# Kernel optimization log

Hardware: AMD Instinct MI355X
Metric: run time of the kernel (lower is better)

## Reference

```python
import jax, jax.numpy as jnp
import numpy as np

N_NODES = 100000
N_EDGES = 3200000
D = 128


def setup_inputs() -> dict:
    key = jax.random.key(0)
    k1, k2, k3, k4, k5 = jax.random.split(key, 5)
    x = jax.random.normal(k1, (N_NODES, D), dtype=jnp.float32)
    weight = jax.random.normal(k2, (D, D), dtype=jnp.float32) * (1.0 / np.sqrt(D))
    bias = jax.random.normal(k3, (D,), dtype=jnp.float32) * 0.01
    edge_weight = jax.random.uniform(k4, (N_EDGES,), dtype=jnp.float32)
    edge_index = jax.random.randint(k5, (2, N_EDGES), 0, N_NODES, dtype=jnp.int64 if jax.config.jax_enable_x64 else jnp.int32)
    return {"x": x, "weight": weight, "bias": bias,
            "edge_weight": edge_weight, "edge_index": edge_index}


def gcn_conv(x, weight, bias, edge_index, edge_weight):
    # PyG GCNConv defaults: normalize=True, add_self_loops=True (fill=1),
    # flow source_to_target: messages gathered from edge_index[0], scattered to edge_index[1].
    n = x.shape[0]
    src, dst = edge_index[0], edge_index[1]
    loop = jnp.arange(n, dtype=src.dtype)
    src = jnp.concatenate([src, loop])
    dst = jnp.concatenate([dst, loop])
    ew = jnp.concatenate([edge_weight, jnp.ones((n,), dtype=edge_weight.dtype)])
    deg = jax.ops.segment_sum(ew, dst, num_segments=n)          # [N]
    dinv = jnp.where(deg > 0, jax.lax.rsqrt(jnp.where(deg > 0, deg, 1.0)), 0.0)
    norm = dinv[src] * ew * dinv[dst]                           # [E+N]
    h = x @ weight.T                                            # [N, D_out]
    msg = h[src] * norm[:, None]                                # gather + scale
    out = jax.ops.segment_sum(msg, dst, num_segments=n)         # scatter-add
    return out + bias


def reference(x, weight, bias, edge_weight, edge_index):
    h = gcn_conv(x, weight, bias, edge_index, edge_weight)
    h = jax.nn.relu(h)            # normalizer is Identity, activation=F.relu
    h = h + x                     # input_dim == output_dim -> projection=Identity
    # dropout: eval mode (deterministic reference) -> no-op
    return h
```

## Files before the change

### kernel.cpp

```cpp
#include <hip/hip_runtime.h>

#define N_NODES 100000
#define N_EDGES 3200000
#define DIM 128

#define NB_C  98
#define CAP_C 36864
#define NB_F  1568
#define CAP_F 2560
#define CAP   96



__device__ __forceinline__ unsigned short f2bf(float f) {
    unsigned u = __float_as_uint(f);
    return (unsigned short)((u + 0x7fffu + ((u >> 16) & 1u)) >> 16);
}


__global__ __launch_bounds__(256) void zero_i_kernel(int* __restrict__ p, int n) {
    int i = blockIdx.x * 256 + threadIdx.x;
    if (i < n) p[i] = 0;
}

__global__ __launch_bounds__(256) void zero_f_kernel(float* __restrict__ p, int n) {
    int i = blockIdx.x * 256 + threadIdx.x;
    if (i < n) p[i] = 0.0f;
}

__global__ __launch_bounds__(256) void zero_u64_kernel(unsigned long long* __restrict__ p, int n) {
    int i = blockIdx.x * 256 + threadIdx.x;
    if (i < n) p[i] = 0ull;
}

__global__ __launch_bounds__(256) void zero_f4_kernel(float4* __restrict__ p, int n4) {
    int i = blockIdx.x * 256 + threadIdx.x;
    if (i < n4) p[i] = make_float4(0.f, 0.f, 0.f, 0.f);
}

__global__ __launch_bounds__(256) void dinv_kernel(float* __restrict__ deg) {
    int i = blockIdx.x * 256 + threadIdx.x;
    if (i < N_NODES) deg[i] = rsqrtf(deg[i] + 1.0f);
}

__global__ __launch_bounds__(256) void dinv_packed_kernel(const unsigned long long* __restrict__ packed,
                                                          float* __restrict__ dinv) {
    int i = blockIdx.x * 256 + threadIdx.x;
    if (i < N_NODES) {
        unsigned long long p = packed[i];
        float deg = (float)(p & 0xFFFFFFFFFFull) * (1.0f / 4294967296.0f);
        dinv[i] = rsqrtf(deg + 1.0f);
    }
}

__global__ __launch_bounds__(256) void wt_kernel(const float* __restrict__ W,
                                                 float* __restrict__ Wt) {
    int idx = blockIdx.x * 256 + threadIdx.x;
    int j = idx >> 7, k = idx & 127;
    Wt[k * 128 + j] = W[idx];
}


__global__ __launch_bounds__(256) void prep_kernel(const float* __restrict__ W,
                                                   float* __restrict__ Wt,
                                                   int* __restrict__ fills) {
    const int b = blockIdx.x;
    const int tid = threadIdx.x;
    if (b < 64) {
        int idx = b * 256 + tid;
        int j = idx >> 7, k = idx & 127;
        Wt[k * 128 + j] = W[idx];
    } else {
        int i = (b - 64) * 256 + tid;
        if (i < NB_C + NB_F) fills[i] = 0;
    }
}


__global__ __launch_bounds__(256) void xscale_kernel(const float4* __restrict__ x4,
                                                     const float* __restrict__ dinv,
                                                     ushort4* __restrict__ xh4) {
    const int i0 = blockIdx.x * 512 + threadIdx.x;
#pragma unroll
    for (int r = 0; r < 2; ++r) {
        int i = i0 + r * 256;
        float di = dinv[i >> 5];
        float4 v = x4[i];
        ushort4 h;
        h.x = f2bf(v.x * di); h.y = f2bf(v.y * di);
        h.z = f2bf(v.z * di); h.w = f2bf(v.w * di);
        xh4[i] = h;
    }
}


__global__ __launch_bounds__(256) void partA1_kernel(const int* __restrict__ ei,
                                                     const float* __restrict__ ew,
                                                     int* __restrict__ fill_c,
                                                     unsigned long long* __restrict__ edc) {
    __shared__ int hist[NB_C];
    __shared__ int base[NB_C];
    const int tid = threadIdx.x;
    const int blockbase = blockIdx.x * 4096;
    for (int i = tid; i < NB_C; i += 256) hist[i] = 0;
    __syncthreads();

    unsigned long long pay[16];
    unsigned meta[16];
#pragma unroll
    for (int i = 0; i < 16; ++i) {
        int e = blockbase + i * 256 + tid;
        meta[i] = 0xFFFFFFFFu;
        if (e < N_EDGES) {
            int src = ei[e];
            int dst = ei[N_EDGES + e];
            float w = ew[e];
            int cb = dst >> 10;
            int pos = atomicAdd(&hist[cb], 1);
            pay[i] = ((unsigned long long)__float_as_uint(w) << 32)
                   | ((unsigned)(dst & 1023) << 17) | (unsigned)src;
            meta[i] = ((unsigned)cb << 16) | (unsigned)pos;
        }
    }
    __syncthreads();
    for (int c = tid; c < NB_C; c += 256) {
        int cnt = hist[c];
        base[c] = (cnt > 0) ? atomicAdd(&fill_c[c], cnt) : 0;
    }
    __syncthreads();
#pragma unroll
    for (int i = 0; i < 16; ++i) {
        if (meta[i] != 0xFFFFFFFFu) {
            int cb = (int)(meta[i] >> 16);
            int pos = base[cb] + (int)(meta[i] & 0xFFFFu);
            if (pos < CAP_C)
                edc[(unsigned)cb * CAP_C + (unsigned)pos] = pay[i];
        }
    }
}


__global__ __launch_bounds__(256) void partA2_kernel(const int* __restrict__ fill_c,
                                                     const unsigned long long* __restrict__ edc,
                                                     int* __restrict__ fill_f,
                                                     unsigned long long* __restrict__ edf) {
    __shared__ int hist[16];
    __shared__ int base[16];
    const int tid = threadIdx.x;
    const int cb = blockIdx.x / 9;
    const int lo = (blockIdx.x % 9) * 4096;
    const int cnt_c = min(fill_c[cb], CAP_C);
    const int hi = min(lo + 4096, cnt_c);
    if (tid < 16) hist[tid] = 0;
    __syncthreads();

    unsigned long long pay[16];
    unsigned meta[16];
#pragma unroll
    for (int i = 0; i < 16; ++i) {
        int idx = lo + i * 256 + tid;
        meta[i] = 0xFFFFFFFFu;
        if (idx < hi) {
            unsigned long long p = edc[(unsigned)cb * CAP_C + (unsigned)idx];
            int f = (int)((p >> 23) & 15);
            int pos = atomicAdd(&hist[f], 1);
            pay[i] = p;
            meta[i] = ((unsigned)f << 16) | (unsigned)pos;
        }
    }
    __syncthreads();
    if (tid < 16) {
        int c = hist[tid];
        base[tid] = (c > 0) ? atomicAdd(&fill_f[cb * 16 + tid], c) : 0;
    }
    __syncthreads();
#pragma unroll
    for (int i = 0; i < 16; ++i) {
        if (meta[i] != 0xFFFFFFFFu) {
            int f = (int)(meta[i] >> 16);
            int pos = base[f] + (int)(meta[i] & 0xFFFFu);
            if (pos < CAP_F)
                edf[((unsigned)(cb * 16 + f)) * CAP_F + (unsigned)pos] = pay[i];
        }
    }
}


__global__ __launch_bounds__(256) void partB_kernel(const int* __restrict__ fill_f,
                                                    unsigned long long* __restrict__ edf,
                                                    float* __restrict__ dinv,
                                                    int* __restrict__ row_start,
                                                    int* __restrict__ row_cnt) {
    __shared__ int hist[64];
    __shared__ float degs[64];
    __shared__ int pref[64];
    const int tid = threadIdx.x;
    const int fb = blockIdx.x;
    const int node_base = (fb >> 4) * 1024 + (fb & 15) * 64;
    const int cnt = min(fill_f[fb], CAP_F);
    if (tid < 64) { hist[tid] = 0; degs[tid] = 0.0f; }
    __syncthreads();

    unsigned long long pay[10];
    unsigned meta[10];
    int m = 0;
    for (int idx = tid; idx < cnt; idx += 256) {
        unsigned long long p = edf[(unsigned)fb * CAP_F + (unsigned)idx];
        int dl = (int)((p >> 17) & 63);
        int pos = atomicAdd(&hist[dl], 1);
        atomicAdd(&degs[dl], __uint_as_float((unsigned)(p >> 32)));
        pay[m] = p;
        meta[m] = ((unsigned)dl << 16) | (unsigned)pos;
        ++m;
    }
    __syncthreads();
    if (tid == 0) {
        int run = 0;
#pragma unroll
        for (int n = 0; n < 64; ++n) { pref[n] = run; run += hist[n]; }
    }
    __syncthreads();
    if (tid < 64) {
        int node = node_base + tid;
        if (node < N_NODES) {
            dinv[node] = rsqrtf(degs[tid] + 1.0f);
            row_start[node] = fb * CAP_F + pref[tid];
            row_cnt[node] = hist[tid];
        }
    }
    for (int i = 0; i < m; ++i) {
        int dl = (int)(meta[i] >> 16);
        edf[(unsigned)fb * CAP_F + (unsigned)(pref[dl] + (int)(meta[i] & 0xFFFFu))] = pay[i];
    }
}


__global__ __launch_bounds__(256) void gatherc_kernel(const int* __restrict__ row_start,
                                                      const int* __restrict__ row_cnt,
                                                      const unsigned long long* __restrict__ edf,
                                                      const float* __restrict__ dinv,
                                                      const unsigned* __restrict__ xh,
                                                      float2* __restrict__ agg2) {
    const int lane = threadIdx.x & 63;
    const int node = blockIdx.x * 4 + (threadIdx.x >> 6);

    const int cnt = row_cnt[node];
    const int start = row_start[node];
    float ax0 = 0.f, ay0 = 0.f, ax1 = 0.f, ay1 = 0.f;

    for (int b = 0; b < cnt; b += 64) {
        int idx = b + lane;
        const bool valid = idx < cnt;
        if (!valid) idx = cnt - 1;
        unsigned long long p = edf[(unsigned)(start + idx)];
        int msrc = (int)(p & 0x1FFFFull);
        float mw = valid ? __uint_as_float((unsigned)(p >> 32)) : 0.0f;
        const int mcnt = min(64, cnt - b);
        const int ng = (mcnt + 7) >> 3;

        unsigned va[8], vb[8];

#define PREF(buf, JB)                                                          \
        _Pragma("unroll")                                                      \
        for (int j = 0; j < 8; ++j) {                                          \
            int s = __builtin_amdgcn_readlane(msrc, (JB) + j);                 \
            buf[j] = xh[(unsigned)s * 64u + (unsigned)lane];                   \
        }
#define CONSUME(buf, JB)                                                       \
        _Pragma("unroll")                                                      \
        for (int j = 0; j < 8; ++j) {                                          \
            float w = __int_as_float(                                          \
                __builtin_amdgcn_readlane(__float_as_int(mw), (JB) + j));      \
            if (j & 1) {                                                       \
                ax1 = fmaf(__uint_as_float(buf[j] << 16), w, ax1);             \
                ay1 = fmaf(__uint_as_float(buf[j] & 0xffff0000u), w, ay1);     \
            } else {                                                           \
                ax0 = fmaf(__uint_as_float(buf[j] << 16), w, ax0);             \
                ay0 = fmaf(__uint_as_float(buf[j] & 0xffff0000u), w, ay0);     \
            }                                                                  \
        }

        PREF(va, 0);
        int g = 0;
        for (; g + 2 < ng; g += 2) {
            PREF(vb, (g + 1) * 8);
            CONSUME(va, g * 8);
            PREF(va, (g + 2) * 8);
            CONSUME(vb, (g + 1) * 8);
        }
        if (g + 1 < ng) {
            PREF(vb, (g + 1) * 8);
            CONSUME(va, g * 8);
            CONSUME(vb, (g + 1) * 8);
        } else {
            CONSUME(va, g * 8);
        }
#undef PREF
#undef CONSUME
    }

    float di = dinv[node];
    agg2[(unsigned)node * 64u + lane] = make_float2((ax0 + ax1) * di, (ay0 + ay1) * di);
}


__global__ __launch_bounds__(256) void bucket_f32_kernel(const int* __restrict__ ei,
                                                         const float* __restrict__ ew,
                                                         unsigned long long* __restrict__ packed,
                                                         int2* __restrict__ ed) {
    int e = blockIdx.x * 256 + threadIdx.x;
    int src = ei[e];
    int dst = ei[N_EDGES + e];
    float w = ew[e];
    unsigned long long inc = (1ull << 40) | (unsigned long long)(w * 4294967296.0f);
    unsigned long long old = atomicAdd(&packed[dst], inc);
    unsigned slot = (unsigned)(old >> 40);
    if (slot < CAP) {
        ed[(unsigned)dst * CAP + slot] = make_int2(src, __float_as_int(w));
    }
}

__global__ __launch_bounds__(256) void gatherb_f32_kernel(const unsigned long long* __restrict__ packed,
                                                          const int2* __restrict__ ed,
                                                          const float* __restrict__ dinv,
                                                          const float2* __restrict__ x2,
                                                          float2* __restrict__ agg2) {
    const int wave = threadIdx.x >> 6;
    const int lane = threadIdx.x & 63;
    const int node = blockIdx.x * 4 + wave;

    int cnt = (int)(packed[node] >> 40);
    cnt = min(cnt, CAP);
    const unsigned base = (unsigned)node * CAP;
    float2 acc = make_float2(0.f, 0.f);

    for (int b = 0; b < cnt; b += 64) {
        int idx = b + lane;
        if (idx >= cnt) idx = cnt - 1;
        int2 my = ed[base + idx];
        float wmy = __int_as_float(my.y) * dinv[my.x];
        int m = min(64, cnt - b);
#pragma unroll 8
        for (int j = 0; j < m; ++j) {
            int s = __builtin_amdgcn_readlane(my.x, j);
            float w = __int_as_float(__builtin_amdgcn_readlane(__float_as_int(wmy), j));
            float2 v = x2[(unsigned)s * 64u + lane];
            acc.x = fmaf(v.x, w, acc.x); acc.y = fmaf(v.y, w, acc.y);
        }
    }
    float di = dinv[node];
    acc.x *= di; acc.y *= di;
    agg2[(unsigned)node * 64u + lane] = acc;
}

__global__ __launch_bounds__(256) void count_deg_kernel(const int* __restrict__ ei,
                                                        const float* __restrict__ ew,
                                                        int* __restrict__ count,
                                                        float* __restrict__ deg) {
    int e = blockIdx.x * 256 + threadIdx.x;
    int dst = ei[N_EDGES + e];
    atomicAdd(&count[dst], 1);
    atomicAdd(&deg[dst], ew[e]);
}

__global__ __launch_bounds__(256) void scatter_kernel(const int* __restrict__ ei,
                                                      const float* __restrict__ ew,
                                                      const float* __restrict__ dinv,
                                                      const float4* __restrict__ x4,
                                                      float* __restrict__ agg) {
    unsigned gid = blockIdx.x * 256u + threadIdx.x;
    unsigned e  = gid >> 5;
    unsigned f4 = gid & 31u;
    int src = ei[e];
    int dst = ei[N_EDGES + e];
    float w = dinv[src] * ew[e] * dinv[dst];
    float4 v = x4[(unsigned)src * 32u + f4];
    float* o = agg + ((unsigned)dst * 128u + f4 * 4u);
    atomicAdd(o + 0, v.x * w);
    atomicAdd(o + 1, v.y * w);
    atomicAdd(o + 2, v.z * w);
    atomicAdd(o + 3, v.w * w);
}


__global__ __launch_bounds__(256) void final_kernel(const float* __restrict__ agg_in,
                                                    const float* __restrict__ x,
                                                    const float* __restrict__ bias,
                                                    const float* __restrict__ dinv,
                                                    const float* __restrict__ Wt,
                                                    float* __restrict__ out) {
    __shared__ float sh_wt[16384];
    const int tid = threadIdx.x;
    {
        const float4* s4 = (const float4*)Wt;
        float4* d4 = (float4*)sh_wt;
#pragma unroll
        for (int i = 0; i < 16; ++i) d4[i * 256 + tid] = s4[i * 256 + tid];
    }
    __syncthreads();

    const int wave = tid >> 6;
    const int lane = tid & 63;
    const int rowbase = blockIdx.x * 32 + wave * 8;

    float areg[16];
#pragma unroll
    for (int r = 0; r < 8; ++r) {
        int row = rowbase + r;
        float di = dinv[row];
        float di2 = di * di;
        int base = row * 128;
        areg[2 * r]     = agg_in[base + lane]      + x[base + lane]      * di2;
        areg[2 * r + 1] = agg_in[base + 64 + lane] + x[base + 64 + lane] * di2;
    }

    float acc0[8], acc1[8];
#pragma unroll
    for (int r = 0; r < 8; ++r) { acc0[r] = 0.f; acc1[r] = 0.f; }

    const float2* wt2 = (const float2*)sh_wt;

#pragma unroll
    for (int kh = 0; kh < 2; ++kh) {
#pragma unroll 16
        for (int kk = 0; kk < 64; ++kk) {
            int k = kh * 64 + kk;
            float2 w = wt2[k * 64 + lane];
#pragma unroll
            for (int r = 0; r < 8; ++r) {
                float ak = __uint_as_float(
                    __builtin_amdgcn_readlane(__float_as_uint(areg[2 * r + kh]), kk));
                acc0[r] = fmaf(ak, w.x, acc0[r]);
                acc1[r] = fmaf(ak, w.y, acc1[r]);
            }
        }
    }

    float2 b = ((const float2*)bias)[lane];
#pragma unroll
    for (int r = 0; r < 8; ++r) {
        int row = rowbase + r;
        float2 xr = ((const float2*)x)[row * 64 + lane];
        float v0 = fmaxf(acc0[r] + b.x, 0.f) + xr.x;
        float v1 = fmaxf(acc1[r] + b.y, 0.f) + xr.y;
        ((float2*)out)[row * 64 + lane] = make_float2(v0, v1);
    }
}


extern "C" void kernel_launch(void* const* d_in, const int* in_sizes, int n_in,
                              void* d_out, int out_size, void* d_ws, size_t ws_size,
                              hipStream_t stream) {
    const float* x    = (const float*)d_in[0];
    const float* W    = (const float*)d_in[1];
    const float* bias = (const float*)d_in[2];
    const float* ew   = (const float*)d_in[3];
    const int*   ei   = (const int*)d_in[4];
    float* out = (float*)d_out;
    char* ws = (char*)d_ws;

    unsigned short* xhA  = (unsigned short*)ws;
    float* WtA       = (float*)(ws + 25600000);
    float* dinvA     = (float*)(ws + 25665536);
    int*   row_start = (int*)  (ws + 26065536);
    int*   row_cnt   = (int*)  (ws + 26465536);
    int*   fill_c    = (int*)  (ws + 26865536);
    int*   fill_f    = fill_c + NB_C;
    unsigned long long* edc = (unsigned long long*)(ws + 26872256);
    unsigned long long* edf = (unsigned long long*)(ws + 55773632);
    const size_t WS_PART = 87886272ull;

    unsigned long long* packed = (unsigned long long*)ws;
    float* dinvB = (float*)(ws + 800000);
    float* WtB   = (float*)(ws + 1200000);
    int2*  edB   = (int2*)(ws + 1265536);
    const size_t WS_BUCKET = 1265536ull + (size_t)N_NODES * CAP * 8ull;

    if (ws_size >= WS_PART) {
        prep_kernel<<<71, 256, 0, stream>>>(W, WtA, fill_c);
        partA1_kernel<<<(N_EDGES + 4095) / 4096, 256, 0, stream>>>(ei, ew, fill_c, edc);
        partA2_kernel<<<NB_C * 9, 256, 0, stream>>>(fill_c, edc, fill_f, edf);
        partB_kernel<<<NB_F, 256, 0, stream>>>(fill_f, edf, dinvA, row_start, row_cnt);
        xscale_kernel<<<6250, 256, 0, stream>>>((const float4*)x, dinvA, (ushort4*)xhA);
        gatherc_kernel<<<N_NODES / 4, 256, 0, stream>>>(row_start, row_cnt, edf, dinvA,
                                                        (const unsigned*)xhA, (float2*)out);
        final_kernel<<<N_NODES / 32, 256, 0, stream>>>(out, x, bias, dinvA, WtA, out);
    } else if (ws_size >= WS_BUCKET) {
        zero_u64_kernel<<<(N_NODES + 255) / 256, 256, 0, stream>>>(packed, N_NODES);
        wt_kernel<<<64, 256, 0, stream>>>(W, WtB);
        bucket_f32_kernel<<<N_EDGES / 256, 256, 0, stream>>>(ei, ew, packed, edB);
        dinv_packed_kernel<<<(N_NODES + 255) / 256, 256, 0, stream>>>(packed, dinvB);
        gatherb_f32_kernel<<<N_NODES / 4, 256, 0, stream>>>(packed, edB, dinvB,
                                                            (const float2*)x, (float2*)out);
        final_kernel<<<N_NODES / 32, 256, 0, stream>>>(out, x, bias, dinvB, WtB, out);
    } else {
        float* deg   = (float*)(ws);
        float* Wt    = (float*)(ws + 400000);
        int*   count = (int*)  (ws + 465536);
        zero_f_kernel<<<(N_NODES + 255) / 256, 256, 0, stream>>>(deg, N_NODES);
        zero_i_kernel<<<(N_NODES + 255) / 256, 256, 0, stream>>>(count, N_NODES);
        wt_kernel<<<64, 256, 0, stream>>>(W, Wt);
        zero_f4_kernel<<<(N_NODES * DIM / 4) / 256, 256, 0, stream>>>((float4*)out,
                                                                      N_NODES * DIM / 4);
        count_deg_kernel<<<N_EDGES / 256, 256, 0, stream>>>(ei, ew, count, deg);
        dinv_kernel<<<(N_NODES + 255) / 256, 256, 0, stream>>>(deg);
        scatter_kernel<<<(N_EDGES / 256) * 32, 256, 0, stream>>>(ei, ew, deg,
                                                                 (const float4*)x, out);
        final_kernel<<<N_NODES / 32, 256, 0, stream>>>(out, x, bias, deg, Wt, out);
    }
}
```

Measured before the change: 397.2 us.

## Partition edges directly into fine buckets and fuse x scaling into partB

Replaces the two-level coarse-then-fine edge partition with a single pass that histograms destinations straight into 1568 fine buckets of 64 nodes, removing the intermediate edc buffer and one full read/write of the edge payload. Fine buckets now map contiguously to nodes (fb*64), and the bf16 scaling of x by dinv moves into partB, so the separate xscale launch goes away. The trade-off is a 1568-entry shared histogram per block, with more global atomics on fill_f and more scattered writes in the partition pass.

Result: slower. 418.5 us (+5.4%).

```diff
diff --git a/kernel.cpp b/kernel.cpp
--- a/kernel.cpp
+++ b/kernel.cpp
@@ -77,32 +77,15 @@
 }
 
 
-__global__ __launch_bounds__(256) void xscale_kernel(const float4* __restrict__ x4,
-                                                     const float* __restrict__ dinv,
-                                                     ushort4* __restrict__ xh4) {
-    const int i0 = blockIdx.x * 512 + threadIdx.x;
-#pragma unroll
-    for (int r = 0; r < 2; ++r) {
-        int i = i0 + r * 256;
-        float di = dinv[i >> 5];
-        float4 v = x4[i];
-        ushort4 h;
-        h.x = f2bf(v.x * di); h.y = f2bf(v.y * di);
-        h.z = f2bf(v.z * di); h.w = f2bf(v.w * di);
-        xh4[i] = h;
-    }
-}
-
-
-__global__ __launch_bounds__(256) void partA1_kernel(const int* __restrict__ ei,
+__global__ __launch_bounds__(256) void partAF_kernel(const int* __restrict__ ei,
                                                      const float* __restrict__ ew,
-                                                     int* __restrict__ fill_c,
-                                                     unsigned long long* __restrict__ edc) {
-    __shared__ int hist[NB_C];
-    __shared__ int base[NB_C];
+                                                     int* __restrict__ fill_f,
+                                                     unsigned long long* __restrict__ edf) {
+    __shared__ int hist[NB_F];
+    __shared__ int base[NB_F];
     const int tid = threadIdx.x;
     const int blockbase = blockIdx.x * 4096;
-    for (int i = tid; i < NB_C; i += 256) hist[i] = 0;
+    for (int i = tid; i < NB_F; i += 256) hist[i] = 0;
     __syncthreads();
 
     unsigned long long pay[16];
@@ -115,63 +98,17 @@
             int src = ei[e];
             int dst = ei[N_EDGES + e];
             float w = ew[e];
-            int cb = dst >> 10;
-            int pos = atomicAdd(&hist[cb], 1);
+            int f = dst >> 6;
+            int pos = atomicAdd(&hist[f], 1);
             pay[i] = ((unsigned long long)__float_as_uint(w) << 32)
                    | ((unsigned)(dst & 1023) << 17) | (unsigned)src;
-            meta[i] = ((unsigned)cb << 16) | (unsigned)pos;
-        }
-    }
-    __syncthreads();
-    for (int c = tid; c < NB_C; c += 256) {
+            meta[i] = ((unsigned)f << 16) | (unsigned)pos;
+        }
+    }
+    __syncthreads();
+    for (int c = tid; c < NB_F; c += 256) {
         int cnt = hist[c];
-        base[c] = (cnt > 0) ? atomicAdd(&fill_c[c], cnt) : 0;
-    }
-    __syncthreads();
-#pragma unroll
-    for (int i = 0; i < 16; ++i) {
-        if (meta[i] != 0xFFFFFFFFu) {
-            int cb = (int)(meta[i] >> 16);
-            int pos = base[cb] + (int)(meta[i] & 0xFFFFu);
-            if (pos < CAP_C)
-                edc[(unsigned)cb * CAP_C + (unsigned)pos] = pay[i];
-        }
-    }
-}
-
-
-__global__ __launch_bounds__(256) void partA2_kernel(const int* __restrict__ fill_c,
-                                                     const unsigned long long* __restrict__ edc,
-                                                     int* __restrict__ fill_f,
-                                                     unsigned long long* __restrict__ edf) {
-    __shared__ int hist[16];
-    __shared__ int base[16];
-    const int tid = threadIdx.x;
-    const int cb = blockIdx.x / 9;
-    const int lo = (blockIdx.x % 9) * 4096;
-    const int cnt_c = min(fill_c[cb], CAP_C);
-    const int hi = min(lo + 4096, cnt_c);
-    if (tid < 16) hist[tid] = 0;
-    __syncthreads();
-
-    unsigned long long pay[16];
-    unsigned meta[16];
-#pragma unroll
-    for (int i = 0; i < 16; ++i) {
-        int idx = lo + i * 256 + tid;
-        meta[i] = 0xFFFFFFFFu;
-        if (idx < hi) {
-            unsigned long long p = edc[(unsigned)cb * CAP_C + (unsigned)idx];
-            int f = (int)((p >> 23) & 15);
-            int pos = atomicAdd(&hist[f], 1);
-            pay[i] = p;
-            meta[i] = ((unsigned)f << 16) | (unsigned)pos;
-        }
-    }
-    __syncthreads();
-    if (tid < 16) {
-        int c = hist[tid];
-        base[tid] = (c > 0) ? atomicAdd(&fill_f[cb * 16 + tid], c) : 0;
+        base[c] = (cnt > 0) ? atomicAdd(&fill_f[c], cnt) : 0;
     }
     __syncthreads();
 #pragma unroll
@@ -180,7 +117,7 @@
             int f = (int)(meta[i] >> 16);
             int pos = base[f] + (int)(meta[i] & 0xFFFFu);
             if (pos < CAP_F)
-                edf[((unsigned)(cb * 16 + f)) * CAP_F + (unsigned)pos] = pay[i];
+                edf[(unsigned)f * CAP_F + (unsigned)pos] = pay[i];
         }
     }
 }
@@ -190,13 +127,15 @@
                                                     unsigned long long* __restrict__ edf,
                                                     float* __restrict__ dinv,
                                                     int* __restrict__ row_start,
-                                                    int* __restrict__ row_cnt) {
+                                                    int* __restrict__ row_cnt,
+                                                    const float4* __restrict__ x4,
+                                                    ushort4* __restrict__ xh4) {
     __shared__ int hist[64];
     __shared__ float degs[64];
     __shared__ int pref[64];
     const int tid = threadIdx.x;
     const int fb = blockIdx.x;
-    const int node_base = (fb >> 4) * 1024 + (fb & 15) * 64;
+    const int node_base = fb * 64;
     const int cnt = min(fill_f[fb], CAP_F);
     if (tid < 64) { hist[tid] = 0; degs[tid] = 0.0f; }
     __syncthreads();
@@ -223,7 +162,9 @@
     if (tid < 64) {
         int node = node_base + tid;
         if (node < N_NODES) {
-            dinv[node] = rsqrtf(degs[tid] + 1.0f);
+            float dv = rsqrtf(degs[tid] + 1.0f);
+            dinv[node] = dv;
+            degs[tid] = dv;
             row_start[node] = fb * CAP_F + pref[tid];
             row_cnt[node] = hist[tid];
         }
@@ -231,6 +172,21 @@
     for (int i = 0; i < m; ++i) {
         int dl = (int)(meta[i] >> 16);
         edf[(unsigned)fb * CAP_F + (unsigned)(pref[dl] + (int)(meta[i] & 0xFFFFu))] = pay[i];
+    }
+    __syncthreads();
+#pragma unroll
+    for (int i = 0; i < 8; ++i) {
+        int idx = i * 256 + tid;
+        int r = idx >> 5;
+        int node = node_base + r;
+        if (node < N_NODES) {
+            float dv = degs[r];
+            float4 v = x4[(unsigned)node * 32u + (unsigned)(idx & 31)];
+            ushort4 h;
+            h.x = f2bf(v.x * dv); h.y = f2bf(v.y * dv);
+            h.z = f2bf(v.z * dv); h.w = f2bf(v.w * dv);
+            xh4[(unsigned)node * 32u + (unsigned)(idx & 31)] = h;
+        }
     }
 }
 
@@ -466,7 +422,6 @@
     int*   row_cnt   = (int*)  (ws + 26465536);
     int*   fill_c    = (int*)  (ws + 26865536);
     int*   fill_f    = fill_c + NB_C;
-    unsigned long long* edc = (unsigned long long*)(ws + 26872256);
     unsigned long long* edf = (unsigned long long*)(ws + 55773632);
     const size_t WS_PART = 87886272ull;
 
@@ -478,10 +433,9 @@
 
     if (ws_size >= WS_PART) {
         prep_kernel<<<71, 256, 0, stream>>>(W, WtA, fill_c);
-        partA1_kernel<<<(N_EDGES + 4095) / 4096, 256, 0, stream>>>(ei, ew, fill_c, edc);
-        partA2_kernel<<<NB_C * 9, 256, 0, stream>>>(fill_c, edc, fill_f, edf);
-        partB_kernel<<<NB_F, 256, 0, stream>>>(fill_f, edf, dinvA, row_start, row_cnt);
-        xscale_kernel<<<6250, 256, 0, stream>>>((const float4*)x, dinvA, (ushort4*)xhA);
+        partAF_kernel<<<(N_EDGES + 4095) / 4096, 256, 0, stream>>>(ei, ew, fill_f, edf);
+        partB_kernel<<<NB_F, 256, 0, stream>>>(fill_f, edf, dinvA, row_start, row_cnt,
+                                               (const float4*)x, (ushort4*)xhA);
         gatherc_kernel<<<N_NODES / 4, 256, 0, stream>>>(row_start, row_cnt, edf, dinvA,
                                                         (const unsigned*)xhA, (float2*)out);
         final_kernel<<<N_NODES / 32, 256, 0, stream>>>(out, x, bias, dinvA, WtA, out);
```

## Fuse x scaling into partB and triple-buffer gather prefetch

Applied to the files above, without the earlier changes.

Removes the separate xscale kernel. Each partB block now scales its own 64 nodes' feature rows by the freshly computed dinv, read from shared memory, and writes the bf16 copy. This saves a launch and a global reread of dinv, at the cost of extra work in partB blocks. The gather kernel moves from double to triple buffering of neighbor row loads, so more loads are in flight, using more registers. The dinv load is hoisted to the kernel start.

New measurement: 394.2 us. Within noise of the previous version (-0.8%).

```diff
diff --git a/kernel.cpp b/kernel.cpp
--- a/kernel.cpp
+++ b/kernel.cpp
@@ -77,23 +77,6 @@
 }
 
 
-__global__ __launch_bounds__(256) void xscale_kernel(const float4* __restrict__ x4,
-                                                     const float* __restrict__ dinv,
-                                                     ushort4* __restrict__ xh4) {
-    const int i0 = blockIdx.x * 512 + threadIdx.x;
-#pragma unroll
-    for (int r = 0; r < 2; ++r) {
-        int i = i0 + r * 256;
-        float di = dinv[i >> 5];
-        float4 v = x4[i];
-        ushort4 h;
-        h.x = f2bf(v.x * di); h.y = f2bf(v.y * di);
-        h.z = f2bf(v.z * di); h.w = f2bf(v.w * di);
-        xh4[i] = h;
-    }
-}
-
-
 __global__ __launch_bounds__(256) void partA1_kernel(const int* __restrict__ ei,
                                                      const float* __restrict__ ew,
                                                      int* __restrict__ fill_c,
@@ -190,13 +173,15 @@
                                                     unsigned long long* __restrict__ edf,
                                                     float* __restrict__ dinv,
                                                     int* __restrict__ row_start,
-                                                    int* __restrict__ row_cnt) {
+                                                    int* __restrict__ row_cnt,
+                                                    const float4* __restrict__ x4,
+                                                    ushort4* __restrict__ xh4) {
     __shared__ int hist[64];
     __shared__ float degs[64];
     __shared__ int pref[64];
     const int tid = threadIdx.x;
     const int fb = blockIdx.x;
-    const int node_base = (fb >> 4) * 1024 + (fb & 15) * 64;
+    const int node_base = fb * 64;
     const int cnt = min(fill_f[fb], CAP_F);
     if (tid < 64) { hist[tid] = 0; degs[tid] = 0.0f; }
     __syncthreads();
@@ -223,7 +208,9 @@
     if (tid < 64) {
         int node = node_base + tid;
         if (node < N_NODES) {
-            dinv[node] = rsqrtf(degs[tid] + 1.0f);
+            float dv = rsqrtf(degs[tid] + 1.0f);
+            dinv[node] = dv;
+            degs[tid] = dv;
             row_start[node] = fb * CAP_F + pref[tid];
             row_cnt[node] = hist[tid];
         }
@@ -231,6 +218,21 @@
     for (int i = 0; i < m; ++i) {
         int dl = (int)(meta[i] >> 16);
         edf[(unsigned)fb * CAP_F + (unsigned)(pref[dl] + (int)(meta[i] & 0xFFFFu))] = pay[i];
+    }
+    __syncthreads();
+#pragma unroll
+    for (int i = 0; i < 8; ++i) {
+        int idx = i * 256 + tid;
+        int r = idx >> 5;
+        int node = node_base + r;
+        if (node < N_NODES) {
+            float dv = degs[r];
+            float4 v = x4[(unsigned)node * 32u + (unsigned)(idx & 31)];
+            ushort4 h;
+            h.x = f2bf(v.x * dv); h.y = f2bf(v.y * dv);
+            h.z = f2bf(v.z * dv); h.w = f2bf(v.w * dv);
+            xh4[(unsigned)node * 32u + (unsigned)(idx & 31)] = h;
+        }
     }
 }
 
@@ -246,6 +248,7 @@
 
     const int cnt = row_cnt[node];
     const int start = row_start[node];
+    const float di = dinv[node];
     float ax0 = 0.f, ay0 = 0.f, ax1 = 0.f, ay1 = 0.f;
 
     for (int b = 0; b < cnt; b += 64) {
@@ -258,7 +261,7 @@
         const int mcnt = min(64, cnt - b);
         const int ng = (mcnt + 7) >> 3;
 
-        unsigned va[8], vb[8];
+        unsigned vA[8], vB[8], vC[8];
 
 #define PREF(buf, JB)                                                          \
         _Pragma("unroll")                                                      \
@@ -280,26 +283,38 @@
             }                                                                  \
         }
 
-        PREF(va, 0);
+        PREF(vA, 0);
+        if (ng > 1) PREF(vB, 8);
         int g = 0;
-        for (; g + 2 < ng; g += 2) {
-            PREF(vb, (g + 1) * 8);
-            CONSUME(va, g * 8);
-            PREF(va, (g + 2) * 8);
-            CONSUME(vb, (g + 1) * 8);
-        }
-        if (g + 1 < ng) {
-            PREF(vb, (g + 1) * 8);
-            CONSUME(va, g * 8);
-            CONSUME(vb, (g + 1) * 8);
+        while (g + 4 < ng) {
+            PREF(vC, (g + 2) * 8);  CONSUME(vA, g * 8);
+            PREF(vA, (g + 3) * 8);  CONSUME(vB, (g + 1) * 8);
+            PREF(vB, (g + 4) * 8);  CONSUME(vC, (g + 2) * 8);
+            g += 3;
+        }
+        const int r = ng - g;
+        if (r == 1) {
+            CONSUME(vA, g * 8);
+        } else if (r == 2) {
+            CONSUME(vA, g * 8);
+            CONSUME(vB, (g + 1) * 8);
+        } else if (r == 3) {
+            PREF(vC, (g + 2) * 8);
+            CONSUME(vA, g * 8);
+            CONSUME(vB, (g + 1) * 8);
+            CONSUME(vC, (g + 2) * 8);
         } else {
-            CONSUME(va, g * 8);
+            PREF(vC, (g + 2) * 8);
+            CONSUME(vA, g * 8);
+            PREF(vA, (g + 3) * 8);
+            CONSUME(vB, (g + 1) * 8);
+            CONSUME(vC, (g + 2) * 8);
+            CONSUME(vA, (g + 3) * 8);
         }
 #undef PREF
 #undef CONSUME
     }
 
-    float di = dinv[node];
     agg2[(unsigned)node * 64u + lane] = make_float2((ax0 + ax1) * di, (ay0 + ay1) * di);
 }
 
@@ -480,8 +495,8 @@
         prep_kernel<<<71, 256, 0, stream>>>(W, WtA, fill_c);
         partA1_kernel<<<(N_EDGES + 4095) / 4096, 256, 0, stream>>>(ei, ew, fill_c, edc);
         partA2_kernel<<<NB_C * 9, 256, 0, stream>>>(fill_c, edc, fill_f, edf);
-        partB_kernel<<<NB_F, 256, 0, stream>>>(fill_f, edf, dinvA, row_start, row_cnt);
-        xscale_kernel<<<6250, 256, 0, stream>>>((const float4*)x, dinvA, (ushort4*)xhA);
+        partB_kernel<<<NB_F, 256, 0, stream>>>(fill_f, edf, dinvA, row_start, row_cnt,
+                                               (const float4*)x, (ushort4*)xhA);
         gatherc_kernel<<<N_NODES / 4, 256, 0, stream>>>(row_start, row_cnt, edf, dinvA,
                                                         (const unsigned*)xhA, (float2*)out);
         final_kernel<<<N_NODES / 32, 256, 0, stream>>>(out, x, bias, dinvA, WtA, out);
```

## Fuse x scaling into partB and sub-sort row edges by source stripe

Applied to the files above, without the earlier changes.

Removes the separate xscale kernel: partB now computes dinv, keeps it in shared memory and writes the dinv-scaled bf16 copy of x for its 64 nodes. This saves one launch and a global re-read of dinv. Within each destination row, edges are also bucketed by source stripe (src>>13) using a 1024-bin histogram, so the gather visits sources in a more clustered order for better cache locality. The cost is more shared-memory use and extra prefix-scan steps in partB, which may lower occupancy.

After: 399.4 us. No clear change (+0.6%).

```diff
diff --git a/kernel.cpp b/kernel.cpp
--- a/kernel.cpp
+++ b/kernel.cpp
@@ -77,23 +77,6 @@
 }
 
 
-__global__ __launch_bounds__(256) void xscale_kernel(const float4* __restrict__ x4,
-                                                     const float* __restrict__ dinv,
-                                                     ushort4* __restrict__ xh4) {
-    const int i0 = blockIdx.x * 512 + threadIdx.x;
-#pragma unroll
-    for (int r = 0; r < 2; ++r) {
-        int i = i0 + r * 256;
-        float di = dinv[i >> 5];
-        float4 v = x4[i];
-        ushort4 h;
-        h.x = f2bf(v.x * di); h.y = f2bf(v.y * di);
-        h.z = f2bf(v.z * di); h.w = f2bf(v.w * di);
-        xh4[i] = h;
-    }
-}
-
-
 __global__ __launch_bounds__(256) void partA1_kernel(const int* __restrict__ ei,
                                                      const float* __restrict__ ew,
                                                      int* __restrict__ fill_c,
@@ -190,15 +173,19 @@
                                                     unsigned long long* __restrict__ edf,
                                                     float* __restrict__ dinv,
                                                     int* __restrict__ row_start,
-                                                    int* __restrict__ row_cnt) {
-    __shared__ int hist[64];
+                                                    int* __restrict__ row_cnt,
+                                                    const float4* __restrict__ x4,
+                                                    ushort4* __restrict__ xh4) {
+    __shared__ int hist[1024];
+    __shared__ int pref[1024];
     __shared__ float degs[64];
-    __shared__ int pref[64];
+    __shared__ int stripe[64];
     const int tid = threadIdx.x;
     const int fb = blockIdx.x;
-    const int node_base = (fb >> 4) * 1024 + (fb & 15) * 64;
+    const int node_base = fb * 64;
     const int cnt = min(fill_f[fb], CAP_F);
-    if (tid < 64) { hist[tid] = 0; degs[tid] = 0.0f; }
+    for (int i = tid; i < 1024; i += 256) hist[i] = 0;
+    if (tid < 64) degs[tid] = 0.0f;
     __syncthreads();
 
     unsigned long long pay[10];
@@ -207,30 +194,64 @@
     for (int idx = tid; idx < cnt; idx += 256) {
         unsigned long long p = edf[(unsigned)fb * CAP_F + (unsigned)idx];
         int dl = (int)((p >> 17) & 63);
-        int pos = atomicAdd(&hist[dl], 1);
+        int src = (int)(p & 0x1FFFFull);
+        int bin = dl * 16 + (src >> 13);
+        int pos = atomicAdd(&hist[bin], 1);
         atomicAdd(&degs[dl], __uint_as_float((unsigned)(p >> 32)));
         pay[m] = p;
-        meta[m] = ((unsigned)dl << 16) | (unsigned)pos;
+        meta[m] = ((unsigned)bin << 16) | (unsigned)pos;
         ++m;
+    }
+    __syncthreads();
+    if (tid < 64) {
+        int s = 0;
+#pragma unroll
+        for (int k = 0; k < 16; ++k) s += hist[tid * 16 + k];
+        stripe[tid] = s;
     }
     __syncthreads();
     if (tid == 0) {
         int run = 0;
 #pragma unroll
-        for (int n = 0; n < 64; ++n) { pref[n] = run; run += hist[n]; }
+        for (int i = 0; i < 64; ++i) { int t = stripe[i]; stripe[i] = run; run += t; }
+    }
+    __syncthreads();
+    if (tid < 64) {
+        int run = stripe[tid];
+#pragma unroll
+        for (int k = 0; k < 16; ++k) { pref[tid * 16 + k] = run; run += hist[tid * 16 + k]; }
     }
     __syncthreads();
     if (tid < 64) {
         int node = node_base + tid;
         if (node < N_NODES) {
-            dinv[node] = rsqrtf(degs[tid] + 1.0f);
-            row_start[node] = fb * CAP_F + pref[tid];
-            row_cnt[node] = hist[tid];
+            float dv = rsqrtf(degs[tid] + 1.0f);
+            dinv[node] = dv;
+            degs[tid] = dv;
+            int s0 = pref[tid * 16];
+            int s1 = (tid < 63) ? pref[(tid + 1) * 16] : cnt;
+            row_start[node] = fb * CAP_F + s0;
+            row_cnt[node] = s1 - s0;
         }
     }
     for (int i = 0; i < m; ++i) {
-        int dl = (int)(meta[i] >> 16);
-        edf[(unsigned)fb * CAP_F + (unsigned)(pref[dl] + (int)(meta[i] & 0xFFFFu))] = pay[i];
+        int bin = (int)(meta[i] >> 16);
+        edf[(unsigned)fb * CAP_F + (unsigned)(pref[bin] + (int)(meta[i] & 0xFFFFu))] = pay[i];
+    }
+    __syncthreads();
+#pragma unroll
+    for (int i = 0; i < 8; ++i) {
+        int idx = i * 256 + tid;
+        int r = idx >> 5;
+        int node = node_base + r;
+        if (node < N_NODES) {
+            float dv = degs[r];
+            float4 v = x4[(unsigned)node * 32u + (unsigned)(idx & 31)];
+            ushort4 h;
+            h.x = f2bf(v.x * dv); h.y = f2bf(v.y * dv);
+            h.z = f2bf(v.z * dv); h.w = f2bf(v.w * dv);
+            xh4[(unsigned)node * 32u + (unsigned)(idx & 31)] = h;
+        }
     }
 }
 
@@ -480,8 +501,8 @@
         prep_kernel<<<71, 256, 0, stream>>>(W, WtA, fill_c);
         partA1_kernel<<<(N_EDGES + 4095) / 4096, 256, 0, stream>>>(ei, ew, fill_c, edc);
         partA2_kernel<<<NB_C * 9, 256, 0, stream>>>(fill_c, edc, fill_f, edf);
-        partB_kernel<<<NB_F, 256, 0, stream>>>(fill_f, edf, dinvA, row_start, row_cnt);
-        xscale_kernel<<<6250, 256, 0, stream>>>((const float4*)x, dinvA, (ushort4*)xhA);
+        partB_kernel<<<NB_F, 256, 0, stream>>>(fill_f, edf, dinvA, row_start, row_cnt,
+                                               (const float4*)x, (ushort4*)xhA);
         gatherc_kernel<<<N_NODES / 4, 256, 0, stream>>>(row_start, row_cnt, edf, dinvA,
                                                         (const unsigned*)xhA, (float2*)out);
         final_kernel<<<N_NODES / 32, 256, 0, stream>>>(out, x, bias, dinvA, WtA, out);
```
